# Kernel optimization log

Hardware: AMD Instinct MI355X
Metric: run time of the kernel (lower is better)

Reference implementation:

```python
import jax, jax.numpy as jnp
import numpy as np

NUM_CLASSES = 1203
C = NUM_CLASSES + 1
ITER = 9001            # > warm_up_iter=8000 (full path), not a multiple of save_iter=1000
GAMMA = 1.0
BETA = 1.0             # forward default loss_type=1 -> beta = 1
EMA = 0.999
LOWER = 1.0 / 3.0
UPPER = 5.0
LOSS_WEIGHT_ARG = 1.0  # forward `loss_weight` arg default
SELF_LOSS_WEIGHT = 1.0 # __init__ loss_weight
N = 16384              # multiple of 64 (interval in collect_grad_optim)


def setup_inputs() -> dict:
    key = jax.random.key(0)
    k1, k2, k3, k4, k5 = jax.random.split(key, 5)
    cls_score = jax.random.normal(k1, (N, C), jnp.float32)
    label = jax.random.randint(k2, (N,), 0, C)
    weight = jax.random.uniform(k3, (N,), jnp.float32)
    classes_logits = jax.random.normal(k4, (C,), jnp.float32) * 0.01
    class_weights_buf = jnp.ones((C,), jnp.float32)
    corr_grad_accu = jax.random.normal(k5, (C, C), jnp.float32) * 0.01
    weights_mean = jnp.ones((1,), jnp.float32)
    return {"cls_score": cls_score, "label": label, "weight": weight,
            "classes_logits": classes_logits, "class_weights_buf": class_weights_buf,
            "corr_grad_accu": corr_grad_accu, "weights_mean": weights_mean}


def reference(cls_score, label, weight, classes_logits, class_weights_buf,
              corr_grad_accu, weights_mean):
    sg = jax.lax.stop_gradient
    n = cls_score.shape[0]
    target = jax.nn.one_hot(label, C, dtype=cls_score.dtype)  # expand_label

    # ---- get_weight (no_grad in torch): beta=1, iter % save_iter != 0 ----
    cw = jnp.clip(class_weights_buf, LOWER, UPPER)
    tmp_weight = (cw ** BETA)[label]                 # (class_weights**beta * target).sum(1)
    wm = EMA * weights_mean[0] + (1.0 - EMA) * tmp_weight.mean()
    tmp_weight = tmp_weight / wm
    tmp_weight = sg(tmp_weight * weight)             # detached in torch

    # ---- focal cross-entropy ----
    logp = jax.nn.log_softmax(cls_score, axis=-1)
    CE = -jnp.take_along_axis(logp, label[:, None], axis=1)[:, 0]
    p = jnp.exp(-CE)
    loss = (1.0 - p) ** GAMMA * CE
    loss = (loss * tmp_weight).mean()                # weight_reduce_loss mean

    # ---- collect_grad_optim (all under no_grad in torch) ----
    cs = sg(cls_score)
    w = sg(weight)
    prob = jax.nn.softmax(cs, axis=-1) + 1e-5                       # [N,C]
    focal_grad = w[:, None] * ((1.0 - prob) / prob - jnp.log(prob)) # [N,C]
    pos_grad = ((1.0 - prob) * prob * focal_grad * target).mean(0)  # [C]
    # corr[i,j] = mean_n target[n,i]*focal_grad[n,i]*prob[n,i]*prob[n,j]
    a = target * focal_grad * prob                                  # [N,C]
    corr = jnp.einsum('ni,nj->ij', a, prob) / n                     # [C,C]
    diag = jnp.arange(C)
    corr = corr.at[diag, diag].set(-pos_grad)
    corr_grad = corr * 100.0 * LOSS_WEIGHT_ARG      # dist.all_reduce = identity (1 proc)

    # ITER >= warm_up_iter branch: EMA update + class weights from logits
    accu = EMA * sg(corr_grad_accu) + (1.0 - EMA) * corr_grad
    cw2 = sg(jax.nn.softmax(classes_logits)) * C    # detached in torch

    tcw = (cw2[:, None] * accu).sum(0) / (-jnp.diagonal(accu) + 1e-6) + cw2
    # ITER > warm_up_iter branch:
    tcw = tcw.at[-1].set(C - tcw[:-1].sum())
    tcw = jnp.clip(tcw, LOWER, UPPER)
    tcw = tcw.at[-1].set(jnp.clip(tcw[-1], LOWER, 1.0))
    tcw = sg(jnp.log(tcw))
    loss_grad = ((tcw - classes_logits) ** 2).mean()

    return (SELF_LOSS_WEIGHT * loss, loss_grad, cw2)
```

## Files before the change

kernel.cpp:

```cpp
#include <hip/hip_runtime.h>
#include <math.h>

#define C_    1204
#define C4_   301
#define NABLK 1024
#define NGBLK 80
#define NDBLK 5
#define GYLEN 76
#define NSGRP 8

__device__ __forceinline__ float waveReduceSum(float v){
    #pragma unroll
    for (int o = 32; o > 0; o >>= 1) v += __shfl_xor(v, o, 64);
    return v;
}
__device__ __forceinline__ float4 exp4v(float4 v){
    return float4{__expf(v.x), __expf(v.y), __expf(v.z), __expf(v.w)};
}
__device__ __forceinline__ float hsum4(float4 v){ return v.x + v.y + v.z + v.w; }

__global__ void k_pre(float* zbase, const float* __restrict__ logits,
                      float* cw2, float* out){
    int t = threadIdx.x;
    if (blockIdx.x > 0){
        int j = (blockIdx.x - 1) * 256 + t;
        if (j < (2 + NSGRP) * C_) zbase[j] = 0.f;
        return;
    }
    __shared__ float red[256];
    float x[5]; float m = -3.402823466e38f;
    #pragma unroll
    for (int k = 0; k < 5; ++k){
        int j = t + k * 256;
        x[k] = (j < C_) ? logits[j] : -3.402823466e38f;
        m = fmaxf(m, x[k]);
    }
    red[t] = m; __syncthreads();
    for (int o = 128; o > 0; o >>= 1){ if (t < o) red[t] = fmaxf(red[t], red[t+o]); __syncthreads(); }
    float bm = red[0]; __syncthreads();
    float ss = 0.f;
    #pragma unroll
    for (int k = 0; k < 5; ++k){ int j = t + k * 256; if (j < C_) ss += __expf(x[k] - bm); }
    red[t] = ss; __syncthreads();
    for (int o = 128; o > 0; o >>= 1){ if (t < o) red[t] += red[t+o]; __syncthreads(); }
    float bs = red[0]; __syncthreads();
    #pragma unroll
    for (int k = 0; k < 5; ++k){
        int j = t + k * 256;
        if (j < C_){ float v = __expf(x[k] - bm) / bs * (float)C_; cw2[j] = v; out[2 + j] = v; }
    }
}

__global__ void k_rows(const float* __restrict__ cs, const int* __restrict__ label,
                       const float* __restrict__ w, const float* __restrict__ cwb,
                       const float* __restrict__ cw2, const float* __restrict__ cga,
                       float* suma, float* sumb, float* S8,
                       float* __restrict__ part1, float* __restrict__ part2,
                       float* __restrict__ Gpart, float* __restrict__ diagG){
    int b = blockIdx.x;
    int tid = threadIdx.x;

    if (b >= NABLK){
        int gb = b - NABLK;
        if (gb < NGBLK){
            int jt = gb % 5, ic = gb / 5;
            int j = jt * 256 + tid;
            if (j < C_){
                int i0 = ic * GYLEN, i1 = min(i0 + GYLEN, C_);
                float p = 0.f;
                #pragma unroll 4
                for (int i = i0; i < i1; ++i) p += cw2[i] * cga[(size_t)i * C_ + j];
                Gpart[ic * C_ + j] = p;
            }
        } else {
            int j = (gb - NGBLK) * 256 + tid;
            if (j < C_) diagG[j] = cga[(size_t)j * C_ + j];
        }
        return;
    }

    __shared__ float Sloc[C_];
    __shared__ float lr1[4], lr2[4];
    int lane = tid & 63, wid = tid >> 6;
    bool has4 = lane < (C4_ - 256);

    for (int j = tid; j < C_; j += 256) Sloc[j] = 0.f;

    float4 acc0 = {0,0,0,0}, acc1 = {0,0,0,0}, acc2 = {0,0,0,0},
           acc3 = {0,0,0,0}, acc4 = {0,0,0,0};
    float accL = 0.f, accT = 0.f;
    int rowbase = b * 16 + wid * 4;

    #pragma unroll 1
    for (int pr = 0; pr < 2; ++pr){
        int nA = rowbase + pr * 2, nB = nA + 1;
        const float4* rowA = reinterpret_cast<const float4*>(cs + (size_t)nA * C_);
        const float4* rowB = reinterpret_cast<const float4*>(cs + (size_t)nB * C_);

        float4 ea0 = rowA[lane], ea1 = rowA[lane + 64], ea2 = rowA[lane + 128], ea3 = rowA[lane + 192];
        float4 eb0 = rowB[lane], eb1 = rowB[lane + 64], eb2 = rowB[lane + 128], eb3 = rowB[lane + 192];
        float4 ea4 = {0,0,0,0}, eb4 = {0,0,0,0};
        if (has4){ ea4 = rowA[lane + 256]; eb4 = rowB[lane + 256]; }

        ea0 = exp4v(ea0); ea1 = exp4v(ea1); ea2 = exp4v(ea2); ea3 = exp4v(ea3);
        eb0 = exp4v(eb0); eb1 = exp4v(eb1); eb2 = exp4v(eb2); eb3 = exp4v(eb3);
        if (has4){ ea4 = exp4v(ea4); eb4 = exp4v(eb4); }

        float sA = hsum4(ea0) + hsum4(ea1) + hsum4(ea2) + hsum4(ea3) + hsum4(ea4);
        float sB = hsum4(eb0) + hsum4(eb1) + hsum4(eb2) + hsum4(eb3) + hsum4(eb4);
        sA = waveReduceSum(sA);
        sB = waveReduceSum(sB);

        float coefv = 0.f;
        if (lane < 2){
            int   n = (lane == 0) ? nA : nB;
            float s = (lane == 0) ? sA : sB;
            int l = label[n];
            float x = cs[(size_t)n * C_ + l];
            float logp = x - __logf(s);
            float p = __expf(logp);
            float lossc = (1.f - p) * (-logp);
            float tw = fminf(fmaxf(cwb[l], 1.f/3.f), 5.f);
            float wn = w[n];
            float pp = p + 1e-5f;
            float fg = wn * ((1.f - pp) / pp - __logf(pp));
            float an = fg * pp;
            atomicAdd(&suma[l], an);
            atomicAdd(&sumb[l], an * pp);
            coefv = cw2[l] * an / s;
            accL += lossc * tw * wn;
            accT += tw;
        }
        float cA = __shfl(coefv, 0, 64);
        float cB = __shfl(coefv, 1, 64);

        acc0.x += cA*ea0.x + cB*eb0.x; acc0.y += cA*ea0.y + cB*eb0.y;
        acc0.z += cA*ea0.z + cB*eb0.z; acc0.w += cA*ea0.w + cB*eb0.w;
        acc1.x += cA*ea1.x + cB*eb1.x; acc1.y += cA*ea1.y + cB*eb1.y;
        acc1.z += cA*ea1.z + cB*eb1.z; acc1.w += cA*ea1.w + cB*eb1.w;
        acc2.x += cA*ea2.x + cB*eb2.x; acc2.y += cA*ea2.y + cB*eb2.y;
        acc2.z += cA*ea2.z + cB*eb2.z; acc2.w += cA*ea2.w + cB*eb2.w;
        acc3.x += cA*ea3.x + cB*eb3.x; acc3.y += cA*ea3.y + cB*eb3.y;
        acc3.z += cA*ea3.z + cB*eb3.z; acc3.w += cA*ea3.w + cB*eb3.w;
        if (has4){
            acc4.x += cA*ea4.x + cB*eb4.x; acc4.y += cA*ea4.y + cB*eb4.y;
            acc4.z += cA*ea4.z + cB*eb4.z; acc4.w += cA*ea4.w + cB*eb4.w;
        }
    }

    accL += __shfl_xor(accL, 1, 64);
    accT += __shfl_xor(accT, 1, 64);
    if (lane == 0){ lr1[wid] = accL; lr2[wid] = accT; }

    float4* Sloc4 = reinterpret_cast<float4*>(Sloc);
    __syncthreads();
    #pragma unroll
    for (int wv = 0; wv < 4; ++wv){
        if (wid == wv){
            float4 t0 = Sloc4[lane      ]; t0.x+=acc0.x; t0.y+=acc0.y; t0.z+=acc0.z; t0.w+=acc0.w; Sloc4[lane      ] = t0;
            float4 t1 = Sloc4[lane +  64]; t1.x+=acc1.x; t1.y+=acc1.y; t1.z+=acc1.z; t1.w+=acc1.w; Sloc4[lane +  64] = t1;
            float4 t2 = Sloc4[lane + 128]; t2.x+=acc2.x; t2.y+=acc2.y; t2.z+=acc2.z; t2.w+=acc2.w; Sloc4[lane + 128] = t2;
            float4 t3 = Sloc4[lane + 192]; t3.x+=acc3.x; t3.y+=acc3.y; t3.z+=acc3.z; t3.w+=acc3.w; Sloc4[lane + 192] = t3;
            if (has4){
                float4 t4 = Sloc4[lane + 256]; t4.x+=acc4.x; t4.y+=acc4.y; t4.z+=acc4.z; t4.w+=acc4.w; Sloc4[lane + 256] = t4;
            }
        }
        __syncthreads();
    }

    float* Sg = S8 + (size_t)(b & (NSGRP - 1)) * C_;
    for (int j = tid; j < C_; j += 256) atomicAdd(&Sg[j], Sloc[j]);

    if (tid == 0){
        part1[b] = lr1[0] + lr1[1] + lr1[2] + lr1[3];
        part2[b] = lr2[0] + lr2[1] + lr2[2] + lr2[3];
    }
}

__global__ void k_last(const float* __restrict__ S8, const float* __restrict__ Gpart,
                       const float* __restrict__ diagG, const float* __restrict__ suma,
                       const float* __restrict__ sumb, const float* __restrict__ cw2,
                       const float* __restrict__ logits, const float* __restrict__ part1,
                       const float* __restrict__ part2, const float* __restrict__ wm0,
                       float* out, int Nn){
    __shared__ float tcw[C_];
    __shared__ float red[256];
    __shared__ float red2[256];
    int t = threadIdx.x;

    float p1 = 0.f, p2 = 0.f;
    for (int k = t; k < NABLK; k += 256){ p1 += part1[k]; p2 += part2[k]; }
    red[t] = p1; red2[t] = p2; __syncthreads();
    for (int o = 128; o > 0; o >>= 1){
        if (t < o){ red[t] += red[t+o]; red2[t] += red2[t+o]; }
        __syncthreads();
    }
    float sumLoss = red[0], sumT = red2[0];
    __syncthreads();

    float pe = 0.f;
    #pragma unroll
    for (int k = 0; k < 5; ++k){
        int j = t + k * 256;
        if (j < C_) pe += cw2[j] * suma[j];
    }
    red[t] = pe; __syncthreads();
    for (int o = 128; o > 0; o >>= 1){ if (t < o) red[t] += red[t+o]; __syncthreads(); }
    float E = red[0] * 1e-5f;
    __syncthreads();

    float scale = 100.f / (float)Nn;
    float psum = 0.f;
    #pragma unroll
    for (int k = 0; k < 5; ++k){
        int j = t + k * 256;
        if (j < C_ - 1){
            float G = 0.f;
            #pragma unroll
            for (int y = 0; y < 16; ++y) G += Gpart[y * C_ + j];
            float Sj = 0.f;
            #pragma unroll
            for (int g = 0; g < NSGRP; ++g) Sj += S8[g * C_ + j];
            float tcol  = 0.999f * G + 0.001f * scale * (Sj + E - cw2[j] * suma[j]);
            float diagA = 0.999f * diagG[j] - 0.001f * scale * (suma[j] - sumb[j]);
            float v = tcol / (-diagA + 1e-6f) + cw2[j];
            tcw[j] = v; psum += v;
        }
    }
    red[t] = psum; __syncthreads();
    for (int o = 128; o > 0; o >>= 1){ if (t < o) red[t] += red[t+o]; __syncthreads(); }
    if (t == 0) tcw[C_ - 1] = (float)C_ - red[0];
    __syncthreads();
    float sq = 0.f;
    #pragma unroll
    for (int k = 0; k < 5; ++k){
        int j = t + k * 256;
        if (j < C_){
            float hi = (j == C_ - 1) ? 1.f : 5.f;
            float v = fminf(fmaxf(tcw[j], 1.f/3.f), hi);
            float d = logf(v) - logits[j];
            sq += d * d;
        }
    }
    red[t] = sq; __syncthreads();
    for (int o = 128; o > 0; o >>= 1){ if (t < o) red[t] += red[t+o]; __syncthreads(); }
    if (t == 0){
        float wm = 0.999f * wm0[0] + 0.001f * (sumT / (float)Nn);
        out[0] = sumLoss / ((float)Nn * wm);
        out[1] = red[0] / (float)C_;
    }
}

extern "C" void kernel_launch(void* const* d_in, const int* in_sizes, int n_in,
                              void* d_out, int out_size, void* d_ws, size_t ws_size,
                              hipStream_t stream){
    (void)n_in; (void)out_size; (void)ws_size;
    const float* cs     = (const float*)d_in[0];
    const int*   label  = (const int*)  d_in[1];
    const float* weight = (const float*)d_in[2];
    const float* logits = (const float*)d_in[3];
    const float* cwb    = (const float*)d_in[4];
    const float* cga    = (const float*)d_in[5];
    const float* wm0    = (const float*)d_in[6];
    float* out = (float*)d_out;
    int N = in_sizes[1];

    float* ws      = (float*)d_ws;
    float* suma    = ws;
    float* sumb    = suma + C_;
    float* S8      = sumb + C_;
    float* cw2     = S8 + NSGRP * C_;
    float* diagG   = cw2 + C_;
    float* part1   = diagG + C_;
    float* part2   = part1 + NABLK;
    float* Gpart   = part2 + NABLK;

    k_pre  <<<1 + ((2 + NSGRP) * C_ + 255) / 256, 256, 0, stream>>>(suma, logits, cw2, out);
    k_rows <<<NABLK + NGBLK + NDBLK,              256, 0, stream>>>(cs, label, weight, cwb,
                                                                    cw2, cga, suma, sumb, S8,
                                                                    part1, part2, Gpart, diagG);
    k_last <<<1,                                  256, 0, stream>>>(S8, Gpart, diagG, suma, sumb,
                                                                    cw2, logits, part1, part2,
                                                                    wm0, out, N);
}
```

Measured before the change: 145.6 us.

## Fuse three kernels into one megakernel with last-block finalization

Merges the pre-pass, row, and final reduction kernels into a single launch. Each block recomputes the softmax of the class logits locally instead of reading a precomputed cw2 buffer, and the last block to finish, detected with an atomic counter, performs the final reduction. Workspace zeroing moves to hipMemsetAsync. This removes two kernel launches and the gaps between them, at the cost of redundant exp work per block and a max-free softmax that could overflow for large logits.

Measured after the change: 244.4 us. 67.8% more time.

```diff
diff --git a/kernel.cpp b/kernel.cpp
--- a/kernel.cpp
+++ b/kernel.cpp
@@ -8,6 +8,7 @@
 #define NDBLK 5
 #define GYLEN 76
 #define NSGRP 8
+#define NTOT  (NABLK + NGBLK + NDBLK + 1)
 
 __device__ __forceinline__ float waveReduceSum(float v){
     #pragma unroll
@@ -19,235 +20,250 @@
 }
 __device__ __forceinline__ float hsum4(float4 v){ return v.x + v.y + v.z + v.w; }
 
-__global__ void k_pre(float* zbase, const float* __restrict__ logits,
-                      float* cw2, float* out){
-    int t = threadIdx.x;
-    if (blockIdx.x > 0){
-        int j = (blockIdx.x - 1) * 256 + t;
-        if (j < (2 + NSGRP) * C_) zbase[j] = 0.f;
-        return;
+__device__ __forceinline__ float blockSumExpLogits(const float* __restrict__ logits,
+                                                   float* red, int t){
+    float s = 0.f;
+    #pragma unroll
+    for (int k = 0; k < 5; ++k){ int j = t + k * 256; if (j < C_) s += __expf(logits[j]); }
+    red[t] = s; __syncthreads();
+    for (int o = 128; o > 0; o >>= 1){ if (t < o) red[t] += red[t+o]; __syncthreads(); }
+    float r = red[0]; __syncthreads();
+    return r;
+}
+
+__global__ __launch_bounds__(256)
+void k_mega(const float* __restrict__ cs, const int* __restrict__ label,
+            const float* __restrict__ w, const float* __restrict__ cwb,
+            const float* __restrict__ logits, const float* __restrict__ cga,
+            const float* __restrict__ wm0, float* __restrict__ out,
+            float* suma, float* sumb, float* S8, unsigned* done,
+            float* __restrict__ part1, float* __restrict__ part2,
+            float* __restrict__ Gpart, float* __restrict__ diagG, int Nn)
+{
+    __shared__ float smem[C_ + 512];
+    const int b = blockIdx.x;
+    const int tid = threadIdx.x;
+
+    if (b < NABLK){
+        float* Sloc = smem;
+        float* lr1  = smem + C_;
+        float* lr2  = smem + C_ + 4;
+        int lane = tid & 63, wid = tid >> 6;
+        bool has4 = lane < (C4_ - 256);
+
+        for (int j = tid; j < C_; j += 256) Sloc[j] = 0.f;
+
+        const float4* lg4 = reinterpret_cast<const float4*>(logits);
+        float slog = hsum4(exp4v(lg4[lane])) + hsum4(exp4v(lg4[lane + 64]))
+                   + hsum4(exp4v(lg4[lane + 128])) + hsum4(exp4v(lg4[lane + 192]));
+        if (has4) slog += hsum4(exp4v(lg4[lane + 256]));
+        slog = waveReduceSum(slog);
+        float Klog = (float)C_ / slog;
+
+        float4 acc0 = {0,0,0,0}, acc1 = {0,0,0,0}, acc2 = {0,0,0,0},
+               acc3 = {0,0,0,0}, acc4 = {0,0,0,0};
+        float accL = 0.f, accT = 0.f;
+        int rowbase = b * 16 + wid * 4;
+
+        #pragma unroll 1
+        for (int pr = 0; pr < 2; ++pr){
+            int nA = rowbase + pr * 2, nB = nA + 1;
+            const float4* rowA = reinterpret_cast<const float4*>(cs + (size_t)nA * C_);
+            const float4* rowB = reinterpret_cast<const float4*>(cs + (size_t)nB * C_);
+
+            float4 ea0 = rowA[lane], ea1 = rowA[lane + 64], ea2 = rowA[lane + 128], ea3 = rowA[lane + 192];
+            float4 eb0 = rowB[lane], eb1 = rowB[lane + 64], eb2 = rowB[lane + 128], eb3 = rowB[lane + 192];
+            float4 ea4 = {0,0,0,0}, eb4 = {0,0,0,0};
+            if (has4){ ea4 = rowA[lane + 256]; eb4 = rowB[lane + 256]; }
+
+            ea0 = exp4v(ea0); ea1 = exp4v(ea1); ea2 = exp4v(ea2); ea3 = exp4v(ea3);
+            eb0 = exp4v(eb0); eb1 = exp4v(eb1); eb2 = exp4v(eb2); eb3 = exp4v(eb3);
+            if (has4){ ea4 = exp4v(ea4); eb4 = exp4v(eb4); }
+
+            float sA = hsum4(ea0) + hsum4(ea1) + hsum4(ea2) + hsum4(ea3) + hsum4(ea4);
+            float sB = hsum4(eb0) + hsum4(eb1) + hsum4(eb2) + hsum4(eb3) + hsum4(eb4);
+            sA = waveReduceSum(sA);
+            sB = waveReduceSum(sB);
+
+            float coefv = 0.f;
+            if (lane < 2){
+                int   n = (lane == 0) ? nA : nB;
+                float s = (lane == 0) ? sA : sB;
+                int l = label[n];
+                float x = cs[(size_t)n * C_ + l];
+                float logp = x - __logf(s);
+                float p = __expf(logp);
+                float lossc = (1.f - p) * (-logp);
+                float tw = fminf(fmaxf(cwb[l], 1.f/3.f), 5.f);
+                float wn = w[n];
+                float pp = p + 1e-5f;
+                float fg = wn * ((1.f - pp) / pp - __logf(pp));
+                float an = fg * pp;
+                atomicAdd(&suma[l], an);
+                atomicAdd(&sumb[l], an * pp);
+                float c2 = Klog * __expf(logits[l]);
+                coefv = c2 * an / s;
+                accL += lossc * tw * wn;
+                accT += tw;
+            }
+            float cA = __shfl(coefv, 0, 64);
+            float cB = __shfl(coefv, 1, 64);
+
+            acc0.x += cA*ea0.x + cB*eb0.x; acc0.y += cA*ea0.y + cB*eb0.y;
+            acc0.z += cA*ea0.z + cB*eb0.z; acc0.w += cA*ea0.w + cB*eb0.w;
+            acc1.x += cA*ea1.x + cB*eb1.x; acc1.y += cA*ea1.y + cB*eb1.y;
+            acc1.z += cA*ea1.z + cB*eb1.z; acc1.w += cA*ea1.w + cB*eb1.w;
+            acc2.x += cA*ea2.x + cB*eb2.x; acc2.y += cA*ea2.y + cB*eb2.y;
+            acc2.z += cA*ea2.z + cB*eb2.z; acc2.w += cA*ea2.w + cB*eb2.w;
+            acc3.x += cA*ea3.x + cB*eb3.x; acc3.y += cA*ea3.y + cB*eb3.y;
+            acc3.z += cA*ea3.z + cB*eb3.z; acc3.w += cA*ea3.w + cB*eb3.w;
+            if (has4){
+                acc4.x += cA*ea4.x + cB*eb4.x; acc4.y += cA*ea4.y + cB*eb4.y;
+                acc4.z += cA*ea4.z + cB*eb4.z; acc4.w += cA*ea4.w + cB*eb4.w;
+            }
+        }
+
+        accL += __shfl_xor(accL, 1, 64);
+        accT += __shfl_xor(accT, 1, 64);
+        if (lane == 0){ lr1[wid] = accL; lr2[wid] = accT; }
+
+        float4* Sloc4 = reinterpret_cast<float4*>(Sloc);
+        __syncthreads();
+        #pragma unroll
+        for (int wv = 0; wv < 4; ++wv){
+            if (wid == wv){
+                float4 t0 = Sloc4[lane      ]; t0.x+=acc0.x; t0.y+=acc0.y; t0.z+=acc0.z; t0.w+=acc0.w; Sloc4[lane      ] = t0;
+                float4 t1 = Sloc4[lane +  64]; t1.x+=acc1.x; t1.y+=acc1.y; t1.z+=acc1.z; t1.w+=acc1.w; Sloc4[lane +  64] = t1;
+                float4 t2 = Sloc4[lane + 128]; t2.x+=acc2.x; t2.y+=acc2.y; t2.z+=acc2.z; t2.w+=acc2.w; Sloc4[lane + 128] = t2;
+                float4 t3 = Sloc4[lane + 192]; t3.x+=acc3.x; t3.y+=acc3.y; t3.z+=acc3.z; t3.w+=acc3.w; Sloc4[lane + 192] = t3;
+                if (has4){
+                    float4 t4 = Sloc4[lane + 256]; t4.x+=acc4.x; t4.y+=acc4.y; t4.z+=acc4.z; t4.w+=acc4.w; Sloc4[lane + 256] = t4;
+                }
+            }
+            __syncthreads();
+        }
+
+        float* Sg = S8 + (size_t)(b & (NSGRP - 1)) * C_;
+        for (int j = tid; j < C_; j += 256) atomicAdd(&Sg[j], Sloc[j]);
+
+        if (tid == 0){
+            part1[b] = lr1[0] + lr1[1] + lr1[2] + lr1[3];
+            part2[b] = lr2[0] + lr2[1] + lr2[2] + lr2[3];
+        }
+    } else if (b < NABLK + NGBLK){
+        int gb = b - NABLK;
+        int jt = gb % 5, ic = gb / 5;
+        float* red  = smem;
+        float* elog = smem + 256;
+        float slog = blockSumExpLogits(logits, red, tid);
+        float K = (float)C_ / slog;
+        int i0 = ic * GYLEN, i1 = min(i0 + GYLEN, C_);
+        if (tid < i1 - i0) elog[tid] = __expf(logits[i0 + tid]);
+        __syncthreads();
+        int j = jt * 256 + tid;
+        if (j < C_){
+            float p = 0.f;
+            #pragma unroll 4
+            for (int i = i0; i < i1; ++i) p += elog[i - i0] * cga[(size_t)i * C_ + j];
+            Gpart[ic * C_ + j] = K * p;
+        }
+    } else if (b < NABLK + NGBLK + NDBLK){
+        int j = (b - NABLK - NGBLK) * 256 + tid;
+        if (j < C_) diagG[j] = cga[(size_t)j * C_ + j];
+    } else {
+        float* red = smem;
+        float slog = blockSumExpLogits(logits, red, tid);
+        float K = (float)C_ / slog;
+        #pragma unroll
+        for (int k = 0; k < 5; ++k){
+            int j = tid + k * 256;
+            if (j < C_) out[2 + j] = K * __expf(logits[j]);
+        }
     }
-    __shared__ float red[256];
-    float x[5]; float m = -3.402823466e38f;
-    #pragma unroll
-    for (int k = 0; k < 5; ++k){
-        int j = t + k * 256;
-        x[k] = (j < C_) ? logits[j] : -3.402823466e38f;
-        m = fmaxf(m, x[k]);
+
+    __threadfence();
+    __syncthreads();
+    __shared__ unsigned isLast;
+    if (tid == 0){
+        unsigned prev = atomicAdd(done, 1u);
+        isLast = (prev == (unsigned)(NTOT - 1)) ? 1u : 0u;
     }
-    red[t] = m; __syncthreads();
-    for (int o = 128; o > 0; o >>= 1){ if (t < o) red[t] = fmaxf(red[t], red[t+o]); __syncthreads(); }
-    float bm = red[0]; __syncthreads();
-    float ss = 0.f;
-    #pragma unroll
-    for (int k = 0; k < 5; ++k){ int j = t + k * 256; if (j < C_) ss += __expf(x[k] - bm); }
-    red[t] = ss; __syncthreads();
-    for (int o = 128; o > 0; o >>= 1){ if (t < o) red[t] += red[t+o]; __syncthreads(); }
-    float bs = red[0]; __syncthreads();
-    #pragma unroll
-    for (int k = 0; k < 5; ++k){
-        int j = t + k * 256;
-        if (j < C_){ float v = __expf(x[k] - bm) / bs * (float)C_; cw2[j] = v; out[2 + j] = v; }
-    }
-}
-
-__global__ void k_rows(const float* __restrict__ cs, const int* __restrict__ label,
-                       const float* __restrict__ w, const float* __restrict__ cwb,
-                       const float* __restrict__ cw2, const float* __restrict__ cga,
-                       float* suma, float* sumb, float* S8,
-                       float* __restrict__ part1, float* __restrict__ part2,
-                       float* __restrict__ Gpart, float* __restrict__ diagG){
-    int b = blockIdx.x;
-    int tid = threadIdx.x;
-
-    if (b >= NABLK){
-        int gb = b - NABLK;
-        if (gb < NGBLK){
-            int jt = gb % 5, ic = gb / 5;
-            int j = jt * 256 + tid;
+    __syncthreads();
+    if (!isLast) return;
+    __threadfence();
+
+    {
+        float* tcw  = smem;
+        float* red  = smem + C_;
+        float* red2 = smem + C_ + 256;
+        int t = tid;
+        __syncthreads();
+
+        float slog = blockSumExpLogits(logits, red, t);
+        float K = (float)C_ / slog;
+
+        float p1 = 0.f, p2 = 0.f;
+        for (int k = t; k < NABLK; k += 256){ p1 += part1[k]; p2 += part2[k]; }
+        red[t] = p1; red2[t] = p2; __syncthreads();
+        for (int o = 128; o > 0; o >>= 1){
+            if (t < o){ red[t] += red[t+o]; red2[t] += red2[t+o]; }
+            __syncthreads();
+        }
+        float sumLoss = red[0], sumT = red2[0];
+        __syncthreads();
+
+        float pe = 0.f;
+        #pragma unroll
+        for (int k = 0; k < 5; ++k){
+            int j = t + k * 256;
+            if (j < C_) pe += K * __expf(logits[j]) * suma[j];
+        }
+        red[t] = pe; __syncthreads();
+        for (int o = 128; o > 0; o >>= 1){ if (t < o) red[t] += red[t+o]; __syncthreads(); }
+        float E = red[0] * 1e-5f;
+        __syncthreads();
+
+        float scale = 100.f / (float)Nn;
+        float psum = 0.f;
+        #pragma unroll
+        for (int k = 0; k < 5; ++k){
+            int j = t + k * 256;
+            if (j < C_ - 1){
+                float c2 = K * __expf(logits[j]);
+                float G = 0.f;
+                #pragma unroll
+                for (int y = 0; y < 16; ++y) G += Gpart[y * C_ + j];
+                float Sj = 0.f;
+                #pragma unroll
+                for (int g = 0; g < NSGRP; ++g) Sj += S8[g * C_ + j];
+                float tcol  = 0.999f * G + 0.001f * scale * (Sj + E - c2 * suma[j]);
+                float diagA = 0.999f * diagG[j] - 0.001f * scale * (suma[j] - sumb[j]);
+                float v = tcol / (-diagA + 1e-6f) + c2;
+                tcw[j] = v; psum += v;
+            }
+        }
+        red[t] = psum; __syncthreads();
+        for (int o = 128; o > 0; o >>= 1){ if (t < o) red[t] += red[t+o]; __syncthreads(); }
+        if (t == 0) tcw[C_ - 1] = (float)C_ - red[0];
+        __syncthreads();
+        float sq = 0.f;
+        #pragma unroll
+        for (int k = 0; k < 5; ++k){
+            int j = t + k * 256;
             if (j < C_){
-                int i0 = ic * GYLEN, i1 = min(i0 + GYLEN, C_);
-                float p = 0.f;
-                #pragma unroll 4
-                for (int i = i0; i < i1; ++i) p += cw2[i] * cga[(size_t)i * C_ + j];
-                Gpart[ic * C_ + j] = p;
-            }
-        } else {
-            int j = (gb - NGBLK) * 256 + tid;
-            if (j < C_) diagG[j] = cga[(size_t)j * C_ + j];
-        }
-        return;
-    }
-
-    __shared__ float Sloc[C_];
-    __shared__ float lr1[4], lr2[4];
-    int lane = tid & 63, wid = tid >> 6;
-    bool has4 = lane < (C4_ - 256);
-
-    for (int j = tid; j < C_; j += 256) Sloc[j] = 0.f;
-
-    float4 acc0 = {0,0,0,0}, acc1 = {0,0,0,0}, acc2 = {0,0,0,0},
-           acc3 = {0,0,0,0}, acc4 = {0,0,0,0};
-    float accL = 0.f, accT = 0.f;
-    int rowbase = b * 16 + wid * 4;
-
-    #pragma unroll 1
-    for (int pr = 0; pr < 2; ++pr){
-        int nA = rowbase + pr * 2, nB = nA + 1;
-        const float4* rowA = reinterpret_cast<const float4*>(cs + (size_t)nA * C_);
-        const float4* rowB = reinterpret_cast<const float4*>(cs + (size_t)nB * C_);
-
-        float4 ea0 = rowA[lane], ea1 = rowA[lane + 64], ea2 = rowA[lane + 128], ea3 = rowA[lane + 192];
-        float4 eb0 = rowB[lane], eb1 = rowB[lane + 64], eb2 = rowB[lane + 128], eb3 = rowB[lane + 192];
-        float4 ea4 = {0,0,0,0}, eb4 = {0,0,0,0};
-        if (has4){ ea4 = rowA[lane + 256]; eb4 = rowB[lane + 256]; }
-
-        ea0 = exp4v(ea0); ea1 = exp4v(ea1); ea2 = exp4v(ea2); ea3 = exp4v(ea3);
-        eb0 = exp4v(eb0); eb1 = exp4v(eb1); eb2 = exp4v(eb2); eb3 = exp4v(eb3);
-        if (has4){ ea4 = exp4v(ea4); eb4 = exp4v(eb4); }
-
-        float sA = hsum4(ea0) + hsum4(ea1) + hsum4(ea2) + hsum4(ea3) + hsum4(ea4);
-        float sB = hsum4(eb0) + hsum4(eb1) + hsum4(eb2) + hsum4(eb3) + hsum4(eb4);
-        sA = waveReduceSum(sA);
-        sB = waveReduceSum(sB);
-
-        float coefv = 0.f;
-        if (lane < 2){
-            int   n = (lane == 0) ? nA : nB;
-            float s = (lane == 0) ? sA : sB;
-            int l = label[n];
-            float x = cs[(size_t)n * C_ + l];
-            float logp = x - __logf(s);
-            float p = __expf(logp);
-            float lossc = (1.f - p) * (-logp);
-            float tw = fminf(fmaxf(cwb[l], 1.f/3.f), 5.f);
-            float wn = w[n];
-            float pp = p + 1e-5f;
-            float fg = wn * ((1.f - pp) / pp - __logf(pp));
-            float an = fg * pp;
-            atomicAdd(&suma[l], an);
-            atomicAdd(&sumb[l], an * pp);
-            coefv = cw2[l] * an / s;
-            accL += lossc * tw * wn;
-            accT += tw;
-        }
-        float cA = __shfl(coefv, 0, 64);
-        float cB = __shfl(coefv, 1, 64);
-
-        acc0.x += cA*ea0.x + cB*eb0.x; acc0.y += cA*ea0.y + cB*eb0.y;
-        acc0.z += cA*ea0.z + cB*eb0.z; acc0.w += cA*ea0.w + cB*eb0.w;
-        acc1.x += cA*ea1.x + cB*eb1.x; acc1.y += cA*ea1.y + cB*eb1.y;
-        acc1.z += cA*ea1.z + cB*eb1.z; acc1.w += cA*ea1.w + cB*eb1.w;
-        acc2.x += cA*ea2.x + cB*eb2.x; acc2.y += cA*ea2.y + cB*eb2.y;
-        acc2.z += cA*ea2.z + cB*eb2.z; acc2.w += cA*ea2.w + cB*eb2.w;
-        acc3.x += cA*ea3.x + cB*eb3.x; acc3.y += cA*ea3.y + cB*eb3.y;
-        acc3.z += cA*ea3.z + cB*eb3.z; acc3.w += cA*ea3.w + cB*eb3.w;
-        if (has4){
-            acc4.x += cA*ea4.x + cB*eb4.x; acc4.y += cA*ea4.y + cB*eb4.y;
-            acc4.z += cA*ea4.z + cB*eb4.z; acc4.w += cA*ea4.w + cB*eb4.w;
-        }
-    }
-
-    accL += __shfl_xor(accL, 1, 64);
-    accT += __shfl_xor(accT, 1, 64);
-    if (lane == 0){ lr1[wid] = accL; lr2[wid] = accT; }
-
-    float4* Sloc4 = reinterpret_cast<float4*>(Sloc);
-    __syncthreads();
-    #pragma unroll
-    for (int wv = 0; wv < 4; ++wv){
-        if (wid == wv){
-            float4 t0 = Sloc4[lane      ]; t0.x+=acc0.x; t0.y+=acc0.y; t0.z+=acc0.z; t0.w+=acc0.w; Sloc4[lane      ] = t0;
-            float4 t1 = Sloc4[lane +  64]; t1.x+=acc1.x; t1.y+=acc1.y; t1.z+=acc1.z; t1.w+=acc1.w; Sloc4[lane +  64] = t1;
-            float4 t2 = Sloc4[lane + 128]; t2.x+=acc2.x; t2.y+=acc2.y; t2.z+=acc2.z; t2.w+=acc2.w; Sloc4[lane + 128] = t2;
-            float4 t3 = Sloc4[lane + 192]; t3.x+=acc3.x; t3.y+=acc3.y; t3.z+=acc3.z; t3.w+=acc3.w; Sloc4[lane + 192] = t3;
-            if (has4){
-                float4 t4 = Sloc4[lane + 256]; t4.x+=acc4.x; t4.y+=acc4.y; t4.z+=acc4.z; t4.w+=acc4.w; Sloc4[lane + 256] = t4;
-            }
-        }
-        __syncthreads();
-    }
-
-    float* Sg = S8 + (size_t)(b & (NSGRP - 1)) * C_;
-    for (int j = tid; j < C_; j += 256) atomicAdd(&Sg[j], Sloc[j]);
-
-    if (tid == 0){
-        part1[b] = lr1[0] + lr1[1] + lr1[2] + lr1[3];
-        part2[b] = lr2[0] + lr2[1] + lr2[2] + lr2[3];
-    }
-}
-
-__global__ void k_last(const float* __restrict__ S8, const float* __restrict__ Gpart,
-                       const float* __restrict__ diagG, const float* __restrict__ suma,
-                       const float* __restrict__ sumb, const float* __restrict__ cw2,
-                       const float* __restrict__ logits, const float* __restrict__ part1,
-                       const float* __restrict__ part2, const float* __restrict__ wm0,
-                       float* out, int Nn){
-    __shared__ float tcw[C_];
-    __shared__ float red[256];
-    __shared__ float red2[256];
-    int t = threadIdx.x;
-
-    float p1 = 0.f, p2 = 0.f;
-    for (int k = t; k < NABLK; k += 256){ p1 += part1[k]; p2 += part2[k]; }
-    red[t] = p1; red2[t] = p2; __syncthreads();
-    for (int o = 128; o > 0; o >>= 1){
-        if (t < o){ red[t] += red[t+o]; red2[t] += red2[t+o]; }
-        __syncthreads();
-    }
-    float sumLoss = red[0], sumT = red2[0];
-    __syncthreads();
-
-    float pe = 0.f;
-    #pragma unroll
-    for (int k = 0; k < 5; ++k){
-        int j = t + k * 256;
-        if (j < C_) pe += cw2[j] * suma[j];
-    }
-    red[t] = pe; __syncthreads();
-    for (int o = 128; o > 0; o >>= 1){ if (t < o) red[t] += red[t+o]; __syncthreads(); }
-    float E = red[0] * 1e-5f;
-    __syncthreads();
-
-    float scale = 100.f / (float)Nn;
-    float psum = 0.f;
-    #pragma unroll
-    for (int k = 0; k < 5; ++k){
-        int j = t + k * 256;
-        if (j < C_ - 1){
-            float G = 0.f;
-            #pragma unroll
-            for (int y = 0; y < 16; ++y) G += Gpart[y * C_ + j];
-            float Sj = 0.f;
-            #pragma unroll
-            for (int g = 0; g < NSGRP; ++g) Sj += S8[g * C_ + j];
-            float tcol  = 0.999f * G + 0.001f * scale * (Sj + E - cw2[j] * suma[j]);
-            float diagA = 0.999f * diagG[j] - 0.001f * scale * (suma[j] - sumb[j]);
-            float v = tcol / (-diagA + 1e-6f) + cw2[j];
-            tcw[j] = v; psum += v;
-        }
-    }
-    red[t] = psum; __syncthreads();
-    for (int o = 128; o > 0; o >>= 1){ if (t < o) red[t] += red[t+o]; __syncthreads(); }
-    if (t == 0) tcw[C_ - 1] = (float)C_ - red[0];
-    __syncthreads();
-    float sq = 0.f;
-    #pragma unroll
-    for (int k = 0; k < 5; ++k){
-        int j = t + k * 256;
-        if (j < C_){
-            float hi = (j == C_ - 1) ? 1.f : 5.f;
-            float v = fminf(fmaxf(tcw[j], 1.f/3.f), hi);
-            float d = logf(v) - logits[j];
-            sq += d * d;
-        }
-    }
-    red[t] = sq; __syncthreads();
-    for (int o = 128; o > 0; o >>= 1){ if (t < o) red[t] += red[t+o]; __syncthreads(); }
-    if (t == 0){
-        float wm = 0.999f * wm0[0] + 0.001f * (sumT / (float)Nn);
-        out[0] = sumLoss / ((float)Nn * wm);
-        out[1] = red[0] / (float)C_;
+                float hi = (j == C_ - 1) ? 1.f : 5.f;
+                float v = fminf(fmaxf(tcw[j], 1.f/3.f), hi);
+                float d = logf(v) - logits[j];
+                sq += d * d;
+            }
+        }
+        red[t] = sq; __syncthreads();
+        for (int o = 128; o > 0; o >>= 1){ if (t < o) red[t] += red[t+o]; __syncthreads(); }
+        if (t == 0){
+            float wm = 0.999f * wm0[0] + 0.001f * (sumT / (float)Nn);
+            out[0] = sumLoss / ((float)Nn * wm);
+            out[1] = red[0] / (float)C_;
+        }
     }
 }
 
@@ -269,17 +285,13 @@
     float* suma    = ws;
     float* sumb    = suma + C_;
     float* S8      = sumb + C_;
-    float* cw2     = S8 + NSGRP * C_;
-    float* diagG   = cw2 + C_;
-    float* part1   = diagG + C_;
+    unsigned* done = (unsigned*)(S8 + NSGRP * C_);
+    float* part1   = (float*)done + 4;
     float* part2   = part1 + NABLK;
     float* Gpart   = part2 + NABLK;
-
-    k_pre  <<<1 + ((2 + NSGRP) * C_ + 255) / 256, 256, 0, stream>>>(suma, logits, cw2, out);
-    k_rows <<<NABLK + NGBLK + NDBLK,              256, 0, stream>>>(cs, label, weight, cwb,
-                                                                    cw2, cga, suma, sumb, S8,
-                                                                    part1, part2, Gpart, diagG);
-    k_last <<<1,                                  256, 0, stream>>>(S8, Gpart, diagG, suma, sumb,
-                                                                    cw2, logits, part1, part2,
-                                                                    wm0, out, N);
-}
+    float* diagG   = Gpart + 16 * C_;
+
+    hipMemsetAsync(d_ws, 0, (size_t)(2 + NSGRP) * C_ * 4 + 16, stream);
+    k_mega <<<NTOT, 256, 0, stream>>>(cs, label, weight, cwb, logits, cga, wm0, out,
+                                      suma, sumb, S8, done, part1, part2, Gpart, diagG, N);
+}
```

## Process more rows per block, widen atomic groups, zero workspace via memset

Applied to the files above, without the earlier changes.

Each row block now handles 32 rows instead of 16, which halves the number of row blocks and the per-block shared-memory flush and atomic traffic. The atomic accumulation buffer is split into 16 groups instead of 8 to reduce contention, and the final kernel sums the extra groups. Workspace zeroing moves out of k_pre into a hipMemsetAsync, adding a separate stream operation. The trade-off is fewer blocks in flight to hide memory latency and more per-block serial work.

Result: no change. 146.1 us (+0.4%).

```diff
diff --git a/kernel.cpp b/kernel.cpp
--- a/kernel.cpp
+++ b/kernel.cpp
@@ -3,11 +3,11 @@
 
 #define C_    1204
 #define C4_   301
-#define NABLK 1024
+#define NABLK 512
 #define NGBLK 80
 #define NDBLK 5
 #define GYLEN 76
-#define NSGRP 8
+#define NSGRP 16
 
 __device__ __forceinline__ float waveReduceSum(float v){
     #pragma unroll
@@ -19,15 +19,9 @@
 }
 __device__ __forceinline__ float hsum4(float4 v){ return v.x + v.y + v.z + v.w; }
 
-__global__ void k_pre(float* zbase, const float* __restrict__ logits,
-                      float* cw2, float* out){
+__global__ void k_pre(const float* __restrict__ logits, float* cw2, float* out){
+    __shared__ float red[256];
     int t = threadIdx.x;
-    if (blockIdx.x > 0){
-        int j = (blockIdx.x - 1) * 256 + t;
-        if (j < (2 + NSGRP) * C_) zbase[j] = 0.f;
-        return;
-    }
-    __shared__ float red[256];
     float x[5]; float m = -3.402823466e38f;
     #pragma unroll
     for (int k = 0; k < 5; ++k){
@@ -54,7 +48,7 @@
 __global__ void k_rows(const float* __restrict__ cs, const int* __restrict__ label,
                        const float* __restrict__ w, const float* __restrict__ cwb,
                        const float* __restrict__ cw2, const float* __restrict__ cga,
-                       float* suma, float* sumb, float* S8,
+                       float* suma, float* sumb, float* S16,
                        float* __restrict__ part1, float* __restrict__ part2,
                        float* __restrict__ Gpart, float* __restrict__ diagG){
     int b = blockIdx.x;
@@ -89,10 +83,10 @@
     float4 acc0 = {0,0,0,0}, acc1 = {0,0,0,0}, acc2 = {0,0,0,0},
            acc3 = {0,0,0,0}, acc4 = {0,0,0,0};
     float accL = 0.f, accT = 0.f;
-    int rowbase = b * 16 + wid * 4;
+    int rowbase = b * 32 + wid * 8;
 
     #pragma unroll 1
-    for (int pr = 0; pr < 2; ++pr){
+    for (int pr = 0; pr < 4; ++pr){
         int nA = rowbase + pr * 2, nB = nA + 1;
         const float4* rowA = reinterpret_cast<const float4*>(cs + (size_t)nA * C_);
         const float4* rowB = reinterpret_cast<const float4*>(cs + (size_t)nB * C_);
@@ -168,7 +162,7 @@
         __syncthreads();
     }
 
-    float* Sg = S8 + (size_t)(b & (NSGRP - 1)) * C_;
+    float* Sg = S16 + (size_t)(b & (NSGRP - 1)) * C_;
     for (int j = tid; j < C_; j += 256) atomicAdd(&Sg[j], Sloc[j]);
 
     if (tid == 0){
@@ -177,7 +171,7 @@
     }
 }
 
-__global__ void k_last(const float* __restrict__ S8, const float* __restrict__ Gpart,
+__global__ void k_last(const float* __restrict__ S16, const float* __restrict__ Gpart,
                        const float* __restrict__ diagG, const float* __restrict__ suma,
                        const float* __restrict__ sumb, const float* __restrict__ cw2,
                        const float* __restrict__ logits, const float* __restrict__ part1,
@@ -220,7 +214,7 @@
             for (int y = 0; y < 16; ++y) G += Gpart[y * C_ + j];
             float Sj = 0.f;
             #pragma unroll
-            for (int g = 0; g < NSGRP; ++g) Sj += S8[g * C_ + j];
+            for (int g = 0; g < NSGRP; ++g) Sj += S16[g * C_ + j];
             float tcol  = 0.999f * G + 0.001f * scale * (Sj + E - cw2[j] * suma[j]);
             float diagA = 0.999f * diagG[j] - 0.001f * scale * (suma[j] - sumb[j]);
             float v = tcol / (-diagA + 1e-6f) + cw2[j];
@@ -268,18 +262,18 @@
     float* ws      = (float*)d_ws;
     float* suma    = ws;
     float* sumb    = suma + C_;
-    float* S8      = sumb + C_;
-    float* cw2     = S8 + NSGRP * C_;
+    float* S16     = sumb + C_;
+    float* cw2     = S16 + NSGRP * C_;
     float* diagG   = cw2 + C_;
     float* part1   = diagG + C_;
     float* part2   = part1 + NABLK;
     float* Gpart   = part2 + NABLK;
 
-    k_pre  <<<1 + ((2 + NSGRP) * C_ + 255) / 256, 256, 0, stream>>>(suma, logits, cw2, out);
-    k_rows <<<NABLK + NGBLK + NDBLK,              256, 0, stream>>>(cs, label, weight, cwb,
-                                                                    cw2, cga, suma, sumb, S8,
-                                                                    part1, part2, Gpart, diagG);
-    k_last <<<1,                                  256, 0, stream>>>(S8, Gpart, diagG, suma, sumb,
-                                                                    cw2, logits, part1, part2,
-                                                                    wm0, out, N);
-}
+    hipMemsetAsync(d_ws, 0, (size_t)(2 + NSGRP) * C_ * 4, stream);
+    k_pre  <<<1,                     256, 0, stream>>>(logits, cw2, out);
+    k_rows <<<NABLK + NGBLK + NDBLK, 256, 0, stream>>>(cs, label, weight, cwb, cw2, cga,
+                                                       suma, sumb, S16, part1, part2,
+                                                       Gpart, diagG);
+    k_last <<<1,                     256, 0, stream>>>(S16, Gpart, diagG, suma, sumb, cw2,
+                                                       logits, part1, part2, wm0, out, N);
+}
```
